# Performance work log

Hardware: AMD Instinct MI355X
Metric: run time of the kernel (lower is better)

Reference implementation:

```python
import jax, jax.numpy as jnp
import numpy as np

B, T, C, H = 4, 1024, 1024, 16
D = C // H
SINK = 4
EPS_LN = 1e-5

def _layernorm(x, w, b):
    mu = jnp.mean(x, axis=-1, keepdims=True)
    var = jnp.mean(jnp.square(x - mu), axis=-1, keepdims=True)
    return (x - mu) * jax.lax.rsqrt(var + EPS_LN) * w + b

def setup_inputs() -> dict:
    key = jax.random.key(0)
    ks = jax.random.split(key, 8)
    s = 0.02
    inp = {
        "x": jax.random.normal(ks[0], (B, T, C), jnp.float32),
        "attention_mask": jnp.ones((B, T), jnp.int32),
        "W_attn": jax.random.normal(ks[1], (C, 3 * C), jnp.float32) * s,
        "b_attn": jnp.zeros((3 * C,), jnp.float32),
        "W_proj": jax.random.normal(ks[2], (C, C), jnp.float32) * s,
        "b_proj": jnp.zeros((C,), jnp.float32),
        "ln1_w": jnp.ones((C,), jnp.float32),
        "ln1_b": jnp.zeros((C,), jnp.float32),
        "ln2_w": jnp.ones((C,), jnp.float32),
        "ln2_b": jnp.zeros((C,), jnp.float32),
        "W_fc": jax.random.normal(ks[3], (C, 4 * C), jnp.float32) * s,
        "b_fc": jnp.zeros((4 * C,), jnp.float32),
        "W_fc2": jax.random.normal(ks[4], (4 * C, C), jnp.float32) * s,
        "b_fc2": jnp.zeros((C,), jnp.float32),
        "threshold": jnp.float32((0 + 1) / 12 * 0.01),  # layer_idx=0, n_layer=12, final_token_threshold=0.01
    }
    return inp

def reference(x, attention_mask, W_attn, b_attn, W_proj, b_proj,
              ln1_w, ln1_b, ln2_w, ln2_b, W_fc, b_fc, W_fc2, b_fc2, threshold):
    # --- attention on ln_1(x), with explicit weight materialization ---
    h = _layernorm(x, ln1_w, ln1_b)
    qkv = h @ W_attn + b_attn                       # (B,T,3C)
    q, k, v = jnp.split(qkv, 3, axis=-1)
    q = q.reshape(B, T, H, D).transpose(0, 2, 1, 3)  # (B,H,T,D)
    k = k.reshape(B, T, H, D).transpose(0, 2, 1, 3)
    v = v.reshape(B, T, H, D).transpose(0, 2, 1, 3)
    scores = jnp.einsum("bhqd,bhkd->bhqk", q, k) * (1.0 / np.sqrt(D))
    causal = jnp.tril(jnp.ones((T, T), bool))[None, None]          # (1,1,T,T)
    keep = causal & (attention_mask[:, None, None, :] != 0)        # (B,1,T,T)
    scores = jnp.where(keep, scores, -jnp.inf)
    att = jax.nn.softmax(scores, axis=-1)
    att = jnp.nan_to_num(att, nan=0.0)              # fully-masked rows -> 0
    y = jnp.einsum("bhqk,bhkd->bhqd", att, v)       # (B,H,T,D)
    y = y.transpose(0, 2, 1, 3).reshape(B, T, C)
    y = y @ W_proj + b_proj                         # dropout=0.0 -> identity

    # --- cumulative-attention importance ---
    imp = att.sum(axis=2).mean(axis=1)              # (B,T): attention received
    pos_norm = jnp.arange(T, 0, -1, dtype=jnp.float32) / T
    imp = imp / (pos_norm[None, :] + 1e-8)
    imp = imp.at[:, :SINK].set(imp.max() + 1.0)

    # --- residual + MLP ---
    x2 = x + y
    m = _layernorm(x2, ln2_w, ln2_b)
    mlp = jax.nn.gelu(m @ W_fc + b_fc, approximate=False) @ W_fc2 + b_fc2
    out = x2 + mlp

    # --- hard pruning mask ---
    mask = (imp >= threshold).astype(jnp.float32)
    mask = mask.at[:, :SINK].set(1.0)
    mask = mask * attention_mask.astype(jnp.float32)
    return out, mask, imp
```

## Files before the change

kernel.cpp:

```cpp
#include <hip/hip_runtime.h>
#include <math.h>

constexpr int Bc = 4, Tc = 1024, Cc = 1024, Hc = 16, Dc = 64, SINKc = 4;
constexpr float EPS_LN = 1e-5f;

typedef __bf16 bf16x4 __attribute__((ext_vector_type(4)));
typedef __bf16 bf16x8 __attribute__((ext_vector_type(8)));
typedef float  f32x4  __attribute__((ext_vector_type(4)));

__global__ __launch_bounds__(256) void transpose_bf16(
    const float* __restrict__ W, __bf16* __restrict__ Wt, int K, int N)
{
    __shared__ float S[32][33];
    int n0 = blockIdx.x * 32, k0 = blockIdx.y * 32;
    int t = threadIdx.x;
    int r = t >> 3, c4 = (t & 7) * 4;
    float4 v = *(const float4*)(W + (size_t)(k0 + r) * N + n0 + c4);
    S[r][c4+0] = v.x; S[r][c4+1] = v.y; S[r][c4+2] = v.z; S[r][c4+3] = v.w;
    __syncthreads();
    bf16x4 o = { (__bf16)S[c4+0][r], (__bf16)S[c4+1][r],
                 (__bf16)S[c4+2][r], (__bf16)S[c4+3][r] };
    *(bf16x4*)(Wt + (size_t)(n0 + r) * K + k0 + c4) = o;
}

__global__ __launch_bounds__(256) void ln_kernel(
    const float* __restrict__ x, const float* __restrict__ w,
    const float* __restrict__ bsh, __bf16* __restrict__ outp)
{
    int row = blockIdx.x;
    const float* xr = x + (size_t)row * Cc;
    int tid = threadIdx.x;

    float4 xl = reinterpret_cast<const float4*>(xr)[tid];
    float s  = xl.x + xl.y + xl.z + xl.w;
    float s2 = xl.x*xl.x + xl.y*xl.y + xl.z*xl.z + xl.w*xl.w;
    for (int off = 32; off; off >>= 1) {
        s  += __shfl_down(s,  off, 64);
        s2 += __shfl_down(s2, off, 64);
    }
    __shared__ float r1[4], r2[4];
    if ((tid & 63) == 0) { r1[tid >> 6] = s; r2[tid >> 6] = s2; }
    __syncthreads();
    float mu  = (r1[0]+r1[1]+r1[2]+r1[3]) * (1.0f / Cc);
    float var = (r2[0]+r2[1]+r2[2]+r2[3]) * (1.0f / Cc) - mu*mu;
    float rstd = rsqrtf(var + EPS_LN);

    float4 wl = reinterpret_cast<const float4*>(w)[tid];
    float4 bl = reinterpret_cast<const float4*>(bsh)[tid];
    bf16x4 o = { (__bf16)((xl.x - mu) * rstd * wl.x + bl.x),
                 (__bf16)((xl.y - mu) * rstd * wl.y + bl.y),
                 (__bf16)((xl.z - mu) * rstd * wl.z + bl.z),
                 (__bf16)((xl.w - mu) * rstd * wl.w + bl.w) };
    *(bf16x4*)(outp + (size_t)row * Cc + tid * 4) = o;
}

template <int EPI, typename OutT, int TM>
__global__ __launch_bounds__(256, 2) void gemm_bf16(
    const __bf16* __restrict__ A, const __bf16* __restrict__ Bt,
    const float* __restrict__ bias, const float* R,
    OutT* Cm, int M, int N, int K)
{
    __shared__ __bf16 As[2][TM * 32];
    __shared__ __bf16 Bs[2][128 * 32];

    const int tid  = threadIdx.x;
    const int wave = tid >> 6, lane = tid & 63;
    const int wm = wave >> 1, wn = wave & 1;
    const int lr = lane & 15, lc = lane >> 4;

    const int gx = N >> 7;
    const int nblk = gridDim.x;
    const int per = nblk >> 3;
    const int rank = (blockIdx.x & 7) * per + (blockIdx.x >> 3);
    const int GM = 8;
    const int grp = rank / (GM * gx);
    const int rem = rank % (GM * gx);
    const int by = grp * GM + (rem % GM);
    const int bx = rem / GM;

    f32x4 acc[TM / 32][4] = {};

    const int srow = lane >> 2;
    const int cphys = lane & 3;

    for (int k0 = 0; k0 < K; k0 += 64) {
        __syncthreads();
        #pragma unroll
        for (int ii = wave; ii < (TM / 16) * 2; ii += 4) {
            int idx = ii >> 1, c = ii & 1;
            int rloc = idx * 16 + srow;
            int clog = (cphys - (rloc >> 1)) & 3;
            const __bf16* ga = A + (size_t)(by * TM + rloc) * K + k0 + c * 32 + clog * 8;
            __builtin_amdgcn_global_load_lds(
                (const __attribute__((address_space(1))) void*)ga,
                (__attribute__((address_space(3))) void*)(&As[c][idx * 512]), 16, 0, 0);
        }
        #pragma unroll
        for (int ii = wave; ii < 16; ii += 4) {
            int idx = ii >> 1, c = ii & 1;
            int rloc = idx * 16 + srow;
            int clog = (cphys - (rloc >> 1)) & 3;
            const __bf16* gb = Bt + (size_t)(bx * 128 + rloc) * K + k0 + c * 32 + clog * 8;
            __builtin_amdgcn_global_load_lds(
                (const __attribute__((address_space(1))) void*)gb,
                (__attribute__((address_space(3))) void*)(&Bs[c][idx * 512]), 16, 0, 0);
        }
        __syncthreads();

        #pragma unroll
        for (int s = 0; s < 2; s++) {
            bf16x8 af[TM / 32], bfr[4];
            #pragma unroll
            for (int i = 0; i < TM / 32; i++) {
                int ra = wm * (TM / 2) + i * 16 + lr;
                int ca = (lc + (ra >> 1)) & 3;
                af[i] = *(const bf16x8*)(&As[s][ra * 32 + ca * 8]);
            }
            #pragma unroll
            for (int j = 0; j < 4; j++) {
                int rb = wn * 64 + j * 16 + lr;
                int cb = (lc + (rb >> 1)) & 3;
                bfr[j] = *(const bf16x8*)(&Bs[s][rb * 32 + cb * 8]);
            }
            #pragma unroll
            for (int i = 0; i < TM / 32; i++)
                #pragma unroll
                for (int j = 0; j < 4; j++)
                    acc[i][j] = __builtin_amdgcn_mfma_f32_16x16x32_bf16(
                        af[i], bfr[j], acc[i][j], 0, 0, 0);
        }
    }

    #pragma unroll
    for (int j = 0; j < 4; j++) {
        int n = bx * 128 + wn * 64 + j * 16 + lr;
        float bv = bias[n];
        #pragma unroll
        for (int i = 0; i < TM / 32; i++) {
            int m0 = by * TM + wm * (TM / 2) + i * 16 + lc * 4;
            #pragma unroll
            for (int e = 0; e < 4; e++) {
                float t = acc[i][j][e] + bv;
                if (EPI == 1) t = 0.5f * t * (1.0f + erff(t * 0.70710678118654752f));
                if (EPI == 2) t += R[(size_t)(m0 + e) * N + n];
                Cm[(size_t)(m0 + e) * N + n] = (OutT)t;
            }
        }
    }
}

__global__ __launch_bounds__(256, 3) void attn_mfma(
    const __bf16* __restrict__ qkv, const int* __restrict__ amask,
    __bf16* __restrict__ ybuf, float* __restrict__ lbuf)
{
    __shared__ __bf16 Kb[2][64 * 32];
    __shared__ __align__(16) __bf16 Vt[64][72];
    __shared__ __align__(16) __bf16 Ps[64][72];

    int blk = blockIdx.x;
    int idx = blk & 15, h = (blk >> 4) & 15, b = blk >> 8;
    int idx2 = (idx + h + b) & 15;
    int p2 = idx2 >> 1;
    int qt = (idx2 & 1) ? p2 : (15 - p2);
    int q0 = qt * 64;

    int tid = threadIdx.x, wave = tid >> 6, lane = tid & 63;
    int quad = lane >> 4, l15 = lane & 15;
    const int srow = lane >> 2, cphys = lane & 3;
    const size_t RS = 3 * Cc;
    const size_t bT = (size_t)b * Tc;

    bf16x8 qf[2];
    {
        const __bf16* qrow = qkv + (bT + q0 + wave * 16 + l15) * RS + h * 64 + quad * 8;
        qf[0] = *(const bf16x8*)qrow;
        qf[1] = *(const bf16x8*)(qrow + 32);
    }

    float l_part[4] = {0.f, 0.f, 0.f, 0.f};
    f32x4 Oacc[4] = {};

    for (int kt = 0; kt <= qt; kt++) {
        int k0 = kt * 64;
        __syncthreads();

        #pragma unroll
        for (int c = 0; c < 2; c++) {
            int rloc = wave * 16 + srow;
            int clog = (cphys - (rloc >> 1)) & 3;
            const __bf16* g = qkv + (bT + k0 + rloc) * RS + Cc + h * 64 + c * 32 + clog * 8;
            __builtin_amdgcn_global_load_lds(
                (const __attribute__((address_space(1))) void*)g,
                (__attribute__((address_space(3))) void*)(&Kb[c][wave * 512]), 16, 0, 0);
        }
        {
            int kk = lane, dbase = wave * 16;
            const __bf16* vrow = qkv + (bT + k0 + kk) * RS + 2 * Cc + h * 64 + dbase;
            bf16x8 v0 = *(const bf16x8*)vrow;
            bf16x8 v1 = *(const bf16x8*)(vrow + 8);
            #pragma unroll
            for (int j = 0; j < 8; j++) Vt[dbase + j][kk] = v0[j];
            #pragma unroll
            for (int j = 0; j < 8; j++) Vt[dbase + 8 + j][kk] = v1[j];
        }
        int am4[4];
        #pragma unroll
        for (int j = 0; j < 4; j++) am4[j] = amask[bT + k0 + j * 16 + l15];
        __syncthreads();

        f32x4 Sacc[4] = {};
        #pragma unroll
        for (int c = 0; c < 2; c++)
            #pragma unroll
            for (int j = 0; j < 4; j++) {
                int rb = j * 16 + l15;
                int cb = (quad + (rb >> 1)) & 3;
                bf16x8 kf = *(const bf16x8*)(&Kb[c][rb * 32 + cb * 8]);
                Sacc[j] = __builtin_amdgcn_mfma_f32_16x16x32_bf16(qf[c], kf, Sacc[j], 0, 0, 0);
            }

        #pragma unroll
        for (int e = 0; e < 4; e++) {
            int qg = q0 + wave * 16 + quad * 4 + e;
            #pragma unroll
            for (int j = 0; j < 4; j++) {
                int kg = k0 + j * 16 + l15;
                float p = (kg <= qg && am4[j] != 0)
                              ? __expf(Sacc[j][e] * 0.125f) : 0.f;
                l_part[e] += p;
                Ps[wave * 16 + quad * 4 + e][j * 16 + l15] = (__bf16)p;
            }
        }
        __syncthreads();

        #pragma unroll
        for (int c2 = 0; c2 < 2; c2++) {
            bf16x8 pa = *(const bf16x8*)(&Ps[wave * 16 + l15][quad * 8 + c2 * 32]);
            #pragma unroll
            for (int j2 = 0; j2 < 4; j2++) {
                bf16x8 vb = *(const bf16x8*)(&Vt[j2 * 16 + l15][quad * 8 + c2 * 32]);
                Oacc[j2] = __builtin_amdgcn_mfma_f32_16x16x32_bf16(pa, vb, Oacc[j2], 0, 0, 0);
            }
        }
    }

    #pragma unroll
    for (int e = 0; e < 4; e++) {
        float l = l_part[e];
        #pragma unroll
        for (int off = 8; off; off >>= 1) l += __shfl_xor(l, off, 64);
        int qg = q0 + wave * 16 + quad * 4 + e;
        float invl = (l > 0.f) ? 1.f / l : 0.f;
        #pragma unroll
        for (int j2 = 0; j2 < 4; j2++)
            ybuf[(bT + qg) * Cc + h * 64 + j2 * 16 + l15] = (__bf16)(Oacc[j2][e] * invl);
        if (l15 == 0)
            lbuf[(size_t)(b * Hc + h) * Tc + qg] = l;
    }
}

__global__ __launch_bounds__(256, 4) void imp_mfma(
    const __bf16* __restrict__ qkv, const int* __restrict__ amask,
    const float* __restrict__ lbuf, float* __restrict__ impbuf)
{
    __shared__ __bf16 Qb[2][64 * 32];
    __shared__ float rls[64];

    int blk = blockIdx.x;
    int idx = blk & 15, h = (blk >> 4) & 15, b = blk >> 8;
    int idx2 = (idx + h + b) & 15;
    int p2 = idx2 >> 1;
    int kt = (idx2 & 1) ? (15 - p2) : p2;
    int k0 = kt * 64;

    int tid = threadIdx.x, wave = tid >> 6, lane = tid & 63;
    int quad = lane >> 4, l15 = lane & 15;
    const int srow = lane >> 2, cphys = lane & 3;
    const size_t RS = 3 * Cc;
    const size_t bT = (size_t)b * Tc;
    const size_t mlrow = (size_t)(b * Hc + h) * Tc;

    bf16x8 kf[2];
    {
        const __bf16* krow = qkv + (bT + k0 + wave * 16 + l15) * RS + Cc + h * 64 + quad * 8;
        kf[0] = *(const bf16x8*)krow;
        kf[1] = *(const bf16x8*)(krow + 32);
    }
    int amk[4];
    #pragma unroll
    for (int e = 0; e < 4; e++) amk[e] = amask[bT + k0 + wave * 16 + quad * 4 + e];

    float sums[4] = {0.f, 0.f, 0.f, 0.f};

    for (int qt = kt; qt < 16; qt++) {
        int q0 = qt * 64;
        __syncthreads();
        #pragma unroll
        for (int c = 0; c < 2; c++) {
            int rloc = wave * 16 + srow;
            int clog = (cphys - (rloc >> 1)) & 3;
            const __bf16* g = qkv + (bT + q0 + rloc) * RS + h * 64 + c * 32 + clog * 8;
            __builtin_amdgcn_global_load_lds(
                (const __attribute__((address_space(1))) void*)g,
                (__attribute__((address_space(3))) void*)(&Qb[c][wave * 512]), 16, 0, 0);
        }
        if (tid < 64) {
            float l = lbuf[mlrow + q0 + tid];
            rls[tid] = (l > 0.f) ? 1.f / l : 0.f;
        }
        __syncthreads();

        f32x4 Sacc[4] = {};
        #pragma unroll
        for (int c = 0; c < 2; c++)
            #pragma unroll
            for (int j = 0; j < 4; j++) {
                int rb = j * 16 + l15;
                int cb = (quad + (rb >> 1)) & 3;
                bf16x8 qb = *(const bf16x8*)(&Qb[c][rb * 32 + cb * 8]);
                Sacc[j] = __builtin_amdgcn_mfma_f32_16x16x32_bf16(kf[c], qb, Sacc[j], 0, 0, 0);
            }

        #pragma unroll
        for (int j = 0; j < 4; j++) {
            int qg = q0 + j * 16 + l15;
            float rl = rls[j * 16 + l15];
            #pragma unroll
            for (int e = 0; e < 4; e++) {
                int kg = k0 + wave * 16 + quad * 4 + e;
                if (kg <= qg && amk[e] != 0 && rl > 0.f)
                    sums[e] += __expf(Sacc[j][e] * 0.125f) * rl;
            }
        }
    }

    #pragma unroll
    for (int e = 0; e < 4; e++) {
        float s = sums[e];
        #pragma unroll
        for (int off = 8; off; off >>= 1) s += __shfl_xor(s, off, 64);
        if (l15 == 0)
            atomicAdd(&impbuf[bT + k0 + wave * 16 + quad * 4 + e], s);
    }
}

__global__ __launch_bounds__(1024) void finalize_kernel(
    const float* __restrict__ impbuf, const int* __restrict__ amask,
    const float* __restrict__ thr, float* __restrict__ out_mask,
    float* __restrict__ out_imp)
{
    __shared__ float red[16];
    int tid = threadIdx.x;
    float vloc[4];
    float gmax = -INFINITY;
    #pragma unroll
    for (int it = 0; it < 4; it++) {
        int i = tid + it * 1024;
        int tt = i % Tc;
        float posn = (float)(Tc - tt) / (float)Tc;
        float v = impbuf[i] * (1.0f / Hc) / (posn + 1e-8f);
        vloc[it] = v;
        gmax = fmaxf(gmax, v);
    }
    for (int off = 32; off; off >>= 1) gmax = fmaxf(gmax, __shfl_down(gmax, off, 64));
    if ((tid & 63) == 0) red[tid >> 6] = gmax;
    __syncthreads();
    float gm = red[0];
    #pragma unroll
    for (int i = 1; i < 16; i++) gm = fmaxf(gm, red[i]);

    float t = thr[0];
    #pragma unroll
    for (int it = 0; it < 4; it++) {
        int i = tid + it * 1024;
        int tt = i % Tc;
        float v = vloc[it];
        if (tt < SINKc) v = gm + 1.0f;
        float mk = (v >= t) ? 1.f : 0.f;
        if (tt < SINKc) mk = 1.f;
        mk *= (float)amask[i];
        out_imp[i]  = v;
        out_mask[i] = mk;
    }
}

extern "C" void kernel_launch(void* const* d_in, const int* in_sizes, int n_in,
                              void* d_out, int out_size, void* d_ws, size_t ws_size,
                              hipStream_t stream)
{
    const float* x      = (const float*)d_in[0];
    const int*   amask  = (const int*)  d_in[1];
    const float* W_attn = (const float*)d_in[2];
    const float* b_attn = (const float*)d_in[3];
    const float* W_proj = (const float*)d_in[4];
    const float* b_proj = (const float*)d_in[5];
    const float* ln1w   = (const float*)d_in[6];
    const float* ln1b   = (const float*)d_in[7];
    const float* ln2w   = (const float*)d_in[8];
    const float* ln2b   = (const float*)d_in[9];
    const float* W_fc   = (const float*)d_in[10];
    const float* b_fc   = (const float*)d_in[11];
    const float* W_fc2  = (const float*)d_in[12];
    const float* b_fc2  = (const float*)d_in[13];
    const float* thr    = (const float*)d_in[14];

    float* out      = (float*)d_out;
    float* out_mask = out + (size_t)Bc * Tc * Cc;
    float* out_imp  = out_mask + (size_t)Bc * Tc;

    char* wsb = (char*)d_ws;
    __bf16* qkvbf = (__bf16*)wsb;
    __bf16* hbf   = (__bf16*)(wsb + 25165824);
    __bf16* ybf   = (__bf16*)(wsb + 33554432);
    __bf16* fcbf  = (__bf16*)(wsb + 41943040);
    __bf16* WaT   = (__bf16*)(wsb + 75497472);
    __bf16* WpT   = (__bf16*)(wsb + 81788928);
    __bf16* WfT   = (__bf16*)(wsb + 83886080);
    __bf16* Wf2T  = (__bf16*)(wsb + 92274688);
    float*  lbuf  = (float*)(wsb + 100663296);
    float*  impb  = (float*)(wsb + 100925440);

    const int M = Bc * Tc;

    transpose_bf16<<<dim3(3*Cc/32, Cc/32), 256, 0, stream>>>(W_attn, WaT, Cc, 3*Cc);
    transpose_bf16<<<dim3(Cc/32,   Cc/32), 256, 0, stream>>>(W_proj, WpT, Cc, Cc);
    transpose_bf16<<<dim3(4*Cc/32, Cc/32), 256, 0, stream>>>(W_fc,   WfT, Cc, 4*Cc);
    transpose_bf16<<<dim3(Cc/32, 4*Cc/32), 256, 0, stream>>>(W_fc2,  Wf2T, 4*Cc, Cc);

    ln_kernel<<<M, 256, 0, stream>>>(x, ln1w, ln1b, hbf);
    gemm_bf16<0, __bf16, 128><<<(3*Cc/128) * (M/128), 256, 0, stream>>>(
        hbf, WaT, b_attn, nullptr, qkvbf, M, 3*Cc, Cc);
    hipMemsetAsync(impb, 0, (size_t)Bc * Tc * sizeof(float), stream);
    attn_mfma<<<Bc * Hc * 16, 256, 0, stream>>>(qkvbf, amask, ybf, lbuf);
    gemm_bf16<2, float, 64><<<(Cc/128) * (M/64), 256, 0, stream>>>(
        ybf, WpT, b_proj, x, out, M, Cc, Cc);
    imp_mfma<<<Bc * Hc * 16, 256, 0, stream>>>(qkvbf, amask, lbuf, impb);
    ln_kernel<<<M, 256, 0, stream>>>(out, ln2w, ln2b, hbf);
    gemm_bf16<1, __bf16, 128><<<(4*Cc/128) * (M/128), 256, 0, stream>>>(
        hbf, WfT, b_fc, nullptr, fcbf, M, 4*Cc, Cc);
    gemm_bf16<2, float, 64><<<(Cc/128) * (M/64), 256, 0, stream>>>(
        fcbf, Wf2T, b_fc2, out, out, M, Cc, 4*Cc);
    finalize_kernel<<<1, 1024, 0, stream>>>(impb, amask, thr, out_mask, out_imp);
}
```

Measured before the change: 369.0 us.

## Double-buffer GEMM LDS tiles to overlap global loads with MFMA compute

The bf16 GEMM now keeps two LDS buffers for the A and B tiles. It issues the global-to-LDS loads for the next K step before running the MFMAs on the current one, and synchronises only once per iteration instead of twice. This is meant to hide global memory latency behind matrix compute. In exchange LDS use per block doubles, and the occupancy hint becomes a template parameter, set to 3 for the 64-row tile variants.

```diff
diff --git a/kernel.cpp b/kernel.cpp
--- a/kernel.cpp
+++ b/kernel.cpp
@@ -54,14 +54,14 @@
     *(bf16x4*)(outp + (size_t)row * Cc + tid * 4) = o;
 }
 
-template <int EPI, typename OutT, int TM>
-__global__ __launch_bounds__(256, 2) void gemm_bf16(
+template <int EPI, typename OutT, int TM, int OCC>
+__global__ __launch_bounds__(256, OCC) void gemm_bf16(
     const __bf16* __restrict__ A, const __bf16* __restrict__ Bt,
     const float* __restrict__ bias, const float* R,
     OutT* Cm, int M, int N, int K)
 {
-    __shared__ __bf16 As[2][TM * 32];
-    __shared__ __bf16 Bs[2][128 * 32];
+    __shared__ __bf16 As[2][2][TM * 32];
+    __shared__ __bf16 Bs[2][2][128 * 32];
 
     const int tid  = threadIdx.x;
     const int wave = tid >> 6, lane = tid & 63;
@@ -83,29 +83,35 @@
     const int srow = lane >> 2;
     const int cphys = lane & 3;
 
-    for (int k0 = 0; k0 < K; k0 += 64) {
-        __syncthreads();
+    auto stage = [&](int buf, int kk) {
         #pragma unroll
         for (int ii = wave; ii < (TM / 16) * 2; ii += 4) {
             int idx = ii >> 1, c = ii & 1;
             int rloc = idx * 16 + srow;
             int clog = (cphys - (rloc >> 1)) & 3;
-            const __bf16* ga = A + (size_t)(by * TM + rloc) * K + k0 + c * 32 + clog * 8;
+            const __bf16* ga = A + (size_t)(by * TM + rloc) * K + kk + c * 32 + clog * 8;
             __builtin_amdgcn_global_load_lds(
                 (const __attribute__((address_space(1))) void*)ga,
-                (__attribute__((address_space(3))) void*)(&As[c][idx * 512]), 16, 0, 0);
+                (__attribute__((address_space(3))) void*)(&As[buf][c][idx * 512]), 16, 0, 0);
         }
         #pragma unroll
         for (int ii = wave; ii < 16; ii += 4) {
             int idx = ii >> 1, c = ii & 1;
             int rloc = idx * 16 + srow;
             int clog = (cphys - (rloc >> 1)) & 3;
-            const __bf16* gb = Bt + (size_t)(bx * 128 + rloc) * K + k0 + c * 32 + clog * 8;
+            const __bf16* gb = Bt + (size_t)(bx * 128 + rloc) * K + kk + c * 32 + clog * 8;
             __builtin_amdgcn_global_load_lds(
                 (const __attribute__((address_space(1))) void*)gb,
-                (__attribute__((address_space(3))) void*)(&Bs[c][idx * 512]), 16, 0, 0);
-        }
-        __syncthreads();
+                (__attribute__((address_space(3))) void*)(&Bs[buf][c][idx * 512]), 16, 0, 0);
+        }
+    };
+
+    stage(0, 0);
+    __syncthreads();
+
+    int cur = 0;
+    for (int k0 = 0; k0 < K; k0 += 64) {
+        if (k0 + 64 < K) stage(cur ^ 1, k0 + 64);
 
         #pragma unroll
         for (int s = 0; s < 2; s++) {
@@ -114,13 +120,13 @@
             for (int i = 0; i < TM / 32; i++) {
                 int ra = wm * (TM / 2) + i * 16 + lr;
                 int ca = (lc + (ra >> 1)) & 3;
-                af[i] = *(const bf16x8*)(&As[s][ra * 32 + ca * 8]);
+                af[i] = *(const bf16x8*)(&As[cur][s][ra * 32 + ca * 8]);
             }
             #pragma unroll
             for (int j = 0; j < 4; j++) {
                 int rb = wn * 64 + j * 16 + lr;
                 int cb = (lc + (rb >> 1)) & 3;
-                bfr[j] = *(const bf16x8*)(&Bs[s][rb * 32 + cb * 8]);
+                bfr[j] = *(const bf16x8*)(&Bs[cur][s][rb * 32 + cb * 8]);
             }
             #pragma unroll
             for (int i = 0; i < TM / 32; i++)
@@ -129,6 +135,9 @@
                     acc[i][j] = __builtin_amdgcn_mfma_f32_16x16x32_bf16(
                         af[i], bfr[j], acc[i][j], 0, 0, 0);
         }
+
+        __syncthreads();
+        cur ^= 1;
     }
 
     #pragma unroll
@@ -428,17 +437,17 @@
     transpose_bf16<<<dim3(Cc/32, 4*Cc/32), 256, 0, stream>>>(W_fc2,  Wf2T, 4*Cc, Cc);
 
     ln_kernel<<<M, 256, 0, stream>>>(x, ln1w, ln1b, hbf);
-    gemm_bf16<0, __bf16, 128><<<(3*Cc/128) * (M/128), 256, 0, stream>>>(
+    gemm_bf16<0, __bf16, 128, 2><<<(3*Cc/128) * (M/128), 256, 0, stream>>>(
         hbf, WaT, b_attn, nullptr, qkvbf, M, 3*Cc, Cc);
     hipMemsetAsync(impb, 0, (size_t)Bc * Tc * sizeof(float), stream);
     attn_mfma<<<Bc * Hc * 16, 256, 0, stream>>>(qkvbf, amask, ybf, lbuf);
-    gemm_bf16<2, float, 64><<<(Cc/128) * (M/64), 256, 0, stream>>>(
+    gemm_bf16<2, float, 64, 3><<<(Cc/128) * (M/64), 256, 0, stream>>>(
         ybf, WpT, b_proj, x, out, M, Cc, Cc);
     imp_mfma<<<Bc * Hc * 16, 256, 0, stream>>>(qkvbf, amask, lbuf, impb);
     ln_kernel<<<M, 256, 0, stream>>>(out, ln2w, ln2b, hbf);
-    gemm_bf16<1, __bf16, 128><<<(4*Cc/128) * (M/128), 256, 0, stream>>>(
+    gemm_bf16<1, __bf16, 128, 2><<<(4*Cc/128) * (M/128), 256, 0, stream>>>(
         hbf, WfT, b_fc, nullptr, fcbf, M, 4*Cc, Cc);
-    gemm_bf16<2, float, 64><<<(Cc/128) * (M/64), 256, 0, stream>>>(
+    gemm_bf16<2, float, 64, 3><<<(Cc/128) * (M/64), 256, 0, stream>>>(
         fcbf, Wf2T, b_fc2, out, out, M, Cc, 4*Cc);
     finalize_kernel<<<1, 1024, 0, stream>>>(impb, amask, thr, out_mask, out_imp);
 }
```

Measured after the change: 389.0 us. 1.05x slower.

## Split-K the N=1024 projection GEMMs with atomic accumulation and raise occupancy

Applied to the files above, without the earlier changes.

The two N=1024 GEMMs (attention projection and FC2) are split in two along K. Each half atomically adds into an output that a new elementwise kernel first fills with residual plus bias. This doubles the block count for these small-N GEMMs to improve CU fill on a many-CU GPU. Launch-bound occupancy hints are also raised (3 for the wide GEMMs, 4 for the split ones). The cost is two extra elementwise passes over the 16MB output, fp32 atomic traffic, and summation order that is no longer deterministic.

```diff
diff --git a/kernel.cpp b/kernel.cpp
--- a/kernel.cpp
+++ b/kernel.cpp
@@ -54,8 +54,20 @@
     *(bf16x4*)(outp + (size_t)row * Cc + tid * 4) = o;
 }
 
-template <int EPI, typename OutT, int TM>
-__global__ __launch_bounds__(256, 2) void gemm_bf16(
+__global__ __launch_bounds__(256) void init_bias_res(
+    const float* __restrict__ R, const float* __restrict__ bias,
+    float* __restrict__ out, int N)
+{
+    int i = blockIdx.x * 256 + threadIdx.x;
+    float4 r = reinterpret_cast<const float4*>(R)[i];
+    int col = (i * 4) & (N - 1);
+    float4 b = *reinterpret_cast<const float4*>(bias + col);
+    float4 o = { r.x + b.x, r.y + b.y, r.z + b.z, r.w + b.w };
+    reinterpret_cast<float4*>(out)[i] = o;
+}
+
+template <int EPI, typename OutT, int TM, int OCC, int SPLITK>
+__global__ __launch_bounds__(256, OCC) void gemm_bf16(
     const __bf16* __restrict__ A, const __bf16* __restrict__ Bt,
     const float* __restrict__ bias, const float* R,
     OutT* Cm, int M, int N, int K)
@@ -72,18 +84,24 @@
     const int nblk = gridDim.x;
     const int per = nblk >> 3;
     const int rank = (blockIdx.x & 7) * per + (blockIdx.x >> 3);
+    const int base = nblk / SPLITK;
+    const int sk = rank / base;
+    const int trank = rank % base;
     const int GM = 8;
-    const int grp = rank / (GM * gx);
-    const int rem = rank % (GM * gx);
+    const int grp = trank / (GM * gx);
+    const int rem = trank % (GM * gx);
     const int by = grp * GM + (rem % GM);
     const int bx = rem / GM;
 
+    const int Kp = K / SPLITK;
+    const int kbeg = sk * Kp, kend = kbeg + Kp;
+
     f32x4 acc[TM / 32][4] = {};
 
     const int srow = lane >> 2;
     const int cphys = lane & 3;
 
-    for (int k0 = 0; k0 < K; k0 += 64) {
+    for (int k0 = kbeg; k0 < kend; k0 += 64) {
         __syncthreads();
         #pragma unroll
         for (int ii = wave; ii < (TM / 16) * 2; ii += 4) {
@@ -134,7 +152,7 @@
     #pragma unroll
     for (int j = 0; j < 4; j++) {
         int n = bx * 128 + wn * 64 + j * 16 + lr;
-        float bv = bias[n];
+        float bv = (EPI == 3) ? 0.f : bias[n];
         #pragma unroll
         for (int i = 0; i < TM / 32; i++) {
             int m0 = by * TM + wm * (TM / 2) + i * 16 + lc * 4;
@@ -143,7 +161,10 @@
                 float t = acc[i][j][e] + bv;
                 if (EPI == 1) t = 0.5f * t * (1.0f + erff(t * 0.70710678118654752f));
                 if (EPI == 2) t += R[(size_t)(m0 + e) * N + n];
-                Cm[(size_t)(m0 + e) * N + n] = (OutT)t;
+                if (EPI == 3)
+                    atomicAdd((float*)&Cm[(size_t)(m0 + e) * N + n], t);
+                else
+                    Cm[(size_t)(m0 + e) * N + n] = (OutT)t;
             }
         }
     }
@@ -428,17 +449,19 @@
     transpose_bf16<<<dim3(Cc/32, 4*Cc/32), 256, 0, stream>>>(W_fc2,  Wf2T, 4*Cc, Cc);
 
     ln_kernel<<<M, 256, 0, stream>>>(x, ln1w, ln1b, hbf);
-    gemm_bf16<0, __bf16, 128><<<(3*Cc/128) * (M/128), 256, 0, stream>>>(
+    gemm_bf16<0, __bf16, 128, 3, 1><<<(3*Cc/128) * (M/128), 256, 0, stream>>>(
         hbf, WaT, b_attn, nullptr, qkvbf, M, 3*Cc, Cc);
     hipMemsetAsync(impb, 0, (size_t)Bc * Tc * sizeof(float), stream);
     attn_mfma<<<Bc * Hc * 16, 256, 0, stream>>>(qkvbf, amask, ybf, lbuf);
-    gemm_bf16<2, float, 64><<<(Cc/128) * (M/64), 256, 0, stream>>>(
-        ybf, WpT, b_proj, x, out, M, Cc, Cc);
+    init_bias_res<<<M * Cc / 4 / 256, 256, 0, stream>>>(x, b_proj, out, Cc);
+    gemm_bf16<3, float, 64, 4, 2><<<2 * (Cc/128) * (M/64), 256, 0, stream>>>(
+        ybf, WpT, b_proj, nullptr, out, M, Cc, Cc);
     imp_mfma<<<Bc * Hc * 16, 256, 0, stream>>>(qkvbf, amask, lbuf, impb);
     ln_kernel<<<M, 256, 0, stream>>>(out, ln2w, ln2b, hbf);
-    gemm_bf16<1, __bf16, 128><<<(4*Cc/128) * (M/128), 256, 0, stream>>>(
+    gemm_bf16<1, __bf16, 128, 3, 1><<<(4*Cc/128) * (M/128), 256, 0, stream>>>(
         hbf, WfT, b_fc, nullptr, fcbf, M, 4*Cc, Cc);
-    gemm_bf16<2, float, 64><<<(Cc/128) * (M/64), 256, 0, stream>>>(
-        fcbf, Wf2T, b_fc2, out, out, M, Cc, 4*Cc);
+    init_bias_res<<<M * Cc / 4 / 256, 256, 0, stream>>>(out, b_fc2, out, Cc);
+    gemm_bf16<3, float, 64, 4, 2><<<2 * (Cc/128) * (M/64), 256, 0, stream>>>(
+        fcbf, Wf2T, b_fc2, nullptr, out, M, Cc, 4*Cc);
     finalize_kernel<<<1, 1024, 0, stream>>>(impb, amask, thr, out_mask, out_imp);
 }
```

Result: slower. 392.6 us (+6.4%).
